# Kernel tuning notes

Hardware: AMD Instinct MI355X
Metric: run time of the kernel (lower is better)

Reference implementation:

```python
import jax, jax.numpy as jnp
import numpy as np

EPS = 1e-5


def setup_inputs() -> dict:
    key = jax.random.key(0)
    ks = jax.random.split(key, 14)
    N, C, H, W, D = 2048, 512, 4, 4, 64
    inp = {
        "x": jax.random.normal(ks[0], (N, C, H, W), jnp.float32),
        "W123": jax.random.normal(ks[1], (3, D, C), jnp.float32) * 0.05,
        "b123": jax.random.normal(ks[2], (3, D), jnp.float32) * 0.05,
        "g123": jax.random.uniform(ks[3], (3, D), jnp.float32, 0.5, 1.5),
        "be123": jax.random.normal(ks[4], (3, D), jnp.float32) * 0.05,
        "m123": jax.random.normal(ks[5], (3, D), jnp.float32) * 0.05,
        "v123": jax.random.uniform(ks[6], (3, D), jnp.float32, 0.5, 1.5),
        "W4": jax.random.normal(ks[7], (C, D), jnp.float32) * 0.05,
        "b4": jax.random.normal(ks[8], (C,), jnp.float32) * 0.05,
        "g4": jax.random.uniform(ks[9], (C,), jnp.float32, 0.5, 1.5),
        "be4": jax.random.normal(ks[10], (C,), jnp.float32) * 0.05,
        "m4": jax.random.normal(ks[11], (C,), jnp.float32) * 0.05,
        "v4": jax.random.uniform(ks[12], (C,), jnp.float32, 0.5, 1.5),
    }
    return inp


def reference(x, W123, b123, g123, be123, m123, v123, W4, b4, g4, be4, m4, v4):
    N, C, H, W = x.shape
    D = W123.shape[1]
    # three parallel 1x1 stride-2 conv branches == strided slice + channel GEMM
    xs = x[:, :, ::2, ::2]                                 # (N, C, H/2, W/2)
    proj = jnp.einsum('nchw,koc->knohw', xs, W123)         # (3, N, D, H/2, W/2)
    bcast = lambda p: p[:, None, :, None, None]
    bn = (proj + bcast(b123) - bcast(m123)) * (bcast(g123) / jnp.sqrt(bcast(v123) + EPS)) + bcast(be123)
    act = jax.nn.relu(bn)                                  # (3, N, D, h, w)
    L = act.shape[-2] * act.shape[-1]
    q = act[0].reshape(N, D, L).transpose(0, 2, 1)         # (N, L, D)
    k = act[1].reshape(N, D, L)                            # (N, D, L)
    v = act[2].reshape(N, D, L).transpose(0, 2, 1)         # (N, L, D)
    attn = jax.nn.softmax(jnp.einsum('nld,ndm->nlm', q, k), axis=2)  # (N, L, L)
    att = jnp.einsum('nlm,nmd->nld', attn, v).transpose(0, 2, 1)     # (N, D, L)
    att = att.reshape(N, D, W, -1)                         # (N, D, W, L//W)
    # conv2: 1x1 conv D->C + BN (no ReLU)
    out2 = jnp.einsum('ndhw,cd->nchw', att, W4) + b4[None, :, None, None]
    cb = lambda p: p[None, :, None, None]
    bn2 = (out2 - cb(m4)) * (cb(g4) / jnp.sqrt(cb(v4) + EPS)) + cb(be4)
    return x + bn2                                         # broadcasts (N,C,4,1) -> (N,C,4,4)
```

## Files before the change

kernel.cpp:

```cpp
#include <hip/hip_runtime.h>
#include <hip/hip_bf16.h>
#include <math.h>

#define EPS 1e-5f

typedef __attribute__((ext_vector_type(8))) short bf8_t;
typedef __attribute__((ext_vector_type(4))) float f4_t;

static __device__ __forceinline__ unsigned short f2b(float f) {
    __hip_bfloat16 h = __float2bfloat16(f);
    return *reinterpret_cast<unsigned short*>(&h);
}


__global__ __launch_bounds__(256) void k0_prep(
    const float* __restrict__ W123, const float* __restrict__ W4,
    const float* __restrict__ b123, const float* __restrict__ g123,
    const float* __restrict__ be123, const float* __restrict__ m123, const float* __restrict__ v123,
    const float* __restrict__ b4, const float* __restrict__ g4,
    const float* __restrict__ be4, const float* __restrict__ m4, const float* __restrict__ v4,
    unsigned short* __restrict__ w1b, unsigned short* __restrict__ w4b,
    float* __restrict__ bn1s, float* __restrict__ bn1h,
    float* __restrict__ bn2s, float* __restrict__ bn2h)
{
    const int bid = blockIdx.x, tid = threadIdx.x;
    if (bid == 64) {
        if (tid < 192) {
            float s = g123[tid] * rsqrtf(v123[tid] + EPS);
            bn1s[tid] = s;
            bn1h[tid] = be123[tid] + (b123[tid] - m123[tid]) * s;
        }
        for (int c = tid; c < 512; c += 256) {
            float s = g4[c] * rsqrtf(v4[c] + EPS);
            bn2s[c] = s;
            bn2h[c] = be4[c] + (b4[c] - m4[c]) * s;
        }
        return;
    }
    const int f = bid * 256 + tid;
    const float* src;
    unsigned short* dst;
    if (f < 12288) {
        int mt = f >> 10, ks = (f >> 6) & 15, lane = f & 63;
        int row = mt * 16 + (lane & 15);
        int k0  = ks * 32 + ((lane >> 4) << 3);
        src = W123 + row * 512 + k0;
        dst = w1b + f * 8;
    } else {
        int f2 = f - 12288;
        int mt = f2 >> 7, ks = (f2 >> 6) & 1, lane = f2 & 63;
        int row = mt * 16 + (lane & 15);
        int k0  = ks * 32 + ((lane >> 4) << 3);
        src = W4 + row * 64 + k0;
        dst = w4b + f2 * 8;
    }
    float4 a = *(const float4*)src;
    float4 b = *(const float4*)(src + 4);
    union { unsigned short u[8]; uint4 v; } o;
    o.u[0]=f2b(a.x); o.u[1]=f2b(a.y); o.u[2]=f2b(a.z); o.u[3]=f2b(a.w);
    o.u[4]=f2b(b.x); o.u[5]=f2b(b.y); o.u[6]=f2b(b.z); o.u[7]=f2b(b.w);
    *(uint4*)dst = o.v;
}

__global__ __launch_bounds__(256, 8) void k1_mfma(
    const float* __restrict__ x,
    const unsigned short* __restrict__ w1b,
    const unsigned short* __restrict__ w4b,
    const float* __restrict__ bn1s, const float* __restrict__ bn1h,
    const float* __restrict__ bn2s, const float* __restrict__ bn2h,
    float* __restrict__ out)
{
    __shared__ __align__(16) char U[8768];
    __shared__ float smx[20];

    unsigned short* Bxs  = (unsigned short*)&U[0];
    float*          actL = (float*)&U[4160];
    unsigned short* B2   = (unsigned short*)&U[0];
    float*          bn2L = (float*)&U[576];

    const int tid = threadIdx.x;
    const int lane = tid & 63, w = tid >> 6;
    const int n = blockIdx.x;
    const float4* x4 = (const float4*)(x + (size_t)n * 8192);
    float4* o4 = (float4*)(out + (size_t)n * 8192);

    #pragma unroll
    for (int k = 0; k < 8; ++k) {
        int f = tid + k * 256;
        float4 v = x4[f];
        int c = f >> 2, j = f & 3;
        if (j == 0) {
            Bxs[0 * 520 + c] = f2b(v.x);
            Bxs[1 * 520 + c] = f2b(v.z);
        } else if (j == 2) {
            Bxs[2 * 520 + c] = f2b(v.x);
            Bxs[3 * 520 + c] = f2b(v.z);
        }
    }
    __syncthreads();

    {
        f4_t acc[3] = {};
        const bf8_t* Af = (const bf8_t*)w1b;
        const int col = lane & 15, kb = (lane >> 4) << 3;
        for (int ks = 0; ks < 16; ++ks) {
            bf8_t bf = *(const bf8_t*)&Bxs[(col & 3) * 520 + ks * 32 + kb];
            #pragma unroll
            for (int mi = 0; mi < 3; ++mi) {
                int mt = w * 3 + mi;
                bf8_t af = Af[(mt * 16 + ks) * 64 + lane];
                acc[mi] = __builtin_amdgcn_mfma_f32_16x16x32_bf16(af, bf, acc[mi], 0, 0, 0);
            }
        }
        if (col < 4) {
            #pragma unroll
            for (int mi = 0; mi < 3; ++mi) {
                int rbase = (w * 3 + mi) * 16 + ((lane >> 4) << 2);
                #pragma unroll
                for (int r = 0; r < 4; ++r) {
                    int row = rbase + r;
                    float v = acc[mi][r] * bn1s[row] + bn1h[row];
                    actL[row * 5 + col] = fmaxf(v, 0.f);
                }
            }
        }
    }
    __syncthreads();

    if (tid < 32) {
        int l = (tid >> 3) & 3, m = (tid >> 1) & 3, dg = tid & 1;
        float part = 0.f;
        #pragma unroll 8
        for (int kk = 0; kk < 32; ++kk) {
            int d = dg * 32 + kk;
            part += actL[d * 5 + l] * actL[(64 + d) * 5 + m];
        }
        part += __shfl_xor(part, 1);
        if (dg == 0) smx[l * 4 + m] = part;
    }
    __syncthreads();

    if (tid < 4) {
        int l = tid;
        float s0 = smx[l*4+0], s1 = smx[l*4+1], s2 = smx[l*4+2], s3 = smx[l*4+3];
        float mx = fmaxf(fmaxf(s0, s1), fmaxf(s2, s3));
        float e0 = expf(s0-mx), e1 = expf(s1-mx), e2 = expf(s2-mx), e3 = expf(s3-mx);
        float inv = 1.f / (e0 + e1 + e2 + e3);
        smx[l*4+0] = e0*inv; smx[l*4+1] = e1*inv;
        smx[l*4+2] = e2*inv; smx[l*4+3] = e3*inv;
    }
    __syncthreads();

    if (tid < 32) {
        int l = tid >> 3, d0 = (tid & 7) * 8;
        float p0 = smx[l*4+0], p1 = smx[l*4+1], p2 = smx[l*4+2], p3 = smx[l*4+3];
        #pragma unroll
        for (int j = 0; j < 8; ++j) {
            int d = d0 + j;
            float sum = p0 * actL[(128+d)*5 + 0] + p1 * actL[(128+d)*5 + 1]
                      + p2 * actL[(128+d)*5 + 2] + p3 * actL[(128+d)*5 + 3];
            B2[l * 72 + d] = f2b(sum);
        }
    }
    __syncthreads();

    {
        const bf8_t* A2f = (const bf8_t*)w4b;
        const int col = lane & 15, kb = (lane >> 4) << 3;
        f4_t acc2[8] = {};
        #pragma unroll
        for (int ks = 0; ks < 2; ++ks) {
            bf8_t bf = *(const bf8_t*)&B2[(col & 3) * 72 + ks * 32 + kb];
            #pragma unroll
            for (int mi = 0; mi < 8; ++mi) {
                int mt = w * 8 + mi;
                bf8_t af = A2f[(mt * 2 + ks) * 64 + lane];
                acc2[mi] = __builtin_amdgcn_mfma_f32_16x16x32_bf16(af, bf, acc2[mi], 0, 0, 0);
            }
        }
        if (col < 4) {
            #pragma unroll
            for (int mi = 0; mi < 8; ++mi) {
                int cbase = (w * 8 + mi) * 16 + ((lane >> 4) << 2);
                #pragma unroll
                for (int r = 0; r < 4; ++r) {
                    int c = cbase + r;
                    bn2L[c * 4 + col] = acc2[mi][r] * bn2s[c] + bn2h[c];
                }
            }
        }
    }
    __syncthreads();

    #pragma unroll
    for (int k = 0; k < 8; ++k) {
        int f = tid + k * 256;
        int c = f >> 2, j = f & 3;
        float b = bn2L[c * 4 + j];
        float4 v = x4[f];
        o4[f] = make_float4(v.x + b, v.y + b, v.z + b, v.w + b);
    }
}

extern "C" void kernel_launch(void* const* d_in, const int* in_sizes, int n_in,
                              void* d_out, int out_size, void* d_ws, size_t ws_size,
                              hipStream_t stream) {
    const float* x     = (const float*)d_in[0];
    const float* W123  = (const float*)d_in[1];
    const float* b123  = (const float*)d_in[2];
    const float* g123  = (const float*)d_in[3];
    const float* be123 = (const float*)d_in[4];
    const float* m123  = (const float*)d_in[5];
    const float* v123  = (const float*)d_in[6];
    const float* W4    = (const float*)d_in[7];
    const float* b4    = (const float*)d_in[8];
    const float* g4    = (const float*)d_in[9];
    const float* be4   = (const float*)d_in[10];
    const float* m4    = (const float*)d_in[11];
    const float* v4    = (const float*)d_in[12];
    float* outp = (float*)d_out;

    char* ws = (char*)d_ws;
    unsigned short* w1b = (unsigned short*)ws;
    unsigned short* w4b = (unsigned short*)(ws + 196608);
    float* bn1s = (float*)(ws + 262144);
    float* bn1h = (float*)(ws + 262912);
    float* bn2s = (float*)(ws + 263680);
    float* bn2h = (float*)(ws + 265728);

    k0_prep<<<65, 256, 0, stream>>>(W123, W4, b123, g123, be123, m123, v123,
                                    b4, g4, be4, m4, v4,
                                    w1b, w4b, bn1s, bn1h, bn2s, bn2h);
    k1_mfma<<<2048, 256, 0, stream>>>(x, w1b, w4b, bn1s, bn1h, bn2s, bn2h, outp);
}
```

Before: 188.1 us.

## Keep x tile in registers and fuse attention softmax phases via shuffles

Each block now loads its x tile into registers once and reuses it for the final residual add instead of re-reading global memory. The score, softmax and weighted-sum phases are merged into one 64-thread wave using shuffles, which removes two block-wide barriers and the shared softmax buffer. Launch bounds drop from 8 to 4 waves per SIMD to leave room for the extra 32 registers, at the cost of lower occupancy. A partial unroll is also added to the first MFMA loop.

```diff
diff --git a/kernel.cpp b/kernel.cpp
--- a/kernel.cpp
+++ b/kernel.cpp
@@ -62,7 +62,7 @@
     *(uint4*)dst = o.v;
 }
 
-__global__ __launch_bounds__(256, 8) void k1_mfma(
+__global__ __launch_bounds__(256, 4) void k1_mfma(
     const float* __restrict__ x,
     const unsigned short* __restrict__ w1b,
     const unsigned short* __restrict__ w4b,
@@ -71,7 +71,6 @@
     float* __restrict__ out)
 {
     __shared__ __align__(16) char U[8768];
-    __shared__ float smx[20];
 
     unsigned short* Bxs  = (unsigned short*)&U[0];
     float*          actL = (float*)&U[4160];
@@ -84,17 +83,27 @@
     const float4* x4 = (const float4*)(x + (size_t)n * 8192);
     float4* o4 = (float4*)(out + (size_t)n * 8192);
 
+    float4 xr[8];
     #pragma unroll
-    for (int k = 0; k < 8; ++k) {
-        int f = tid + k * 256;
-        float4 v = x4[f];
-        int c = f >> 2, j = f & 3;
+    for (int k = 0; k < 8; ++k) xr[k] = x4[tid + k * 256];
+
+    {
+        const int j = tid & 3;
+        const int cb = tid >> 2;
         if (j == 0) {
-            Bxs[0 * 520 + c] = f2b(v.x);
-            Bxs[1 * 520 + c] = f2b(v.z);
+            #pragma unroll
+            for (int k = 0; k < 8; ++k) {
+                int c = cb + k * 64;
+                Bxs[0 * 520 + c] = f2b(xr[k].x);
+                Bxs[1 * 520 + c] = f2b(xr[k].z);
+            }
         } else if (j == 2) {
-            Bxs[2 * 520 + c] = f2b(v.x);
-            Bxs[3 * 520 + c] = f2b(v.z);
+            #pragma unroll
+            for (int k = 0; k < 8; ++k) {
+                int c = cb + k * 64;
+                Bxs[2 * 520 + c] = f2b(xr[k].x);
+                Bxs[3 * 520 + c] = f2b(xr[k].z);
+            }
         }
     }
     __syncthreads();
@@ -103,6 +112,7 @@
         f4_t acc[3] = {};
         const bf8_t* Af = (const bf8_t*)w1b;
         const int col = lane & 15, kb = (lane >> 4) << 3;
+        #pragma unroll 4
         for (int ks = 0; ks < 16; ++ks) {
             bf8_t bf = *(const bf8_t*)&Bxs[(col & 3) * 520 + ks * 32 + kb];
             #pragma unroll
@@ -127,39 +137,34 @@
     }
     __syncthreads();
 
-    if (tid < 32) {
-        int l = (tid >> 3) & 3, m = (tid >> 1) & 3, dg = tid & 1;
+    if (tid < 64) {
+        int i = (tid & 31) >> 1, dg = tid & 1;
+        int sl = i >> 2, sm = i & 3;
         float part = 0.f;
         #pragma unroll 8
         for (int kk = 0; kk < 32; ++kk) {
             int d = dg * 32 + kk;
-            part += actL[d * 5 + l] * actL[(64 + d) * 5 + m];
+            part += actL[d * 5 + sl] * actL[(64 + d) * 5 + sm];
         }
         part += __shfl_xor(part, 1);
-        if (dg == 0) smx[l * 4 + m] = part;
-    }
-    __syncthreads();
-
-    if (tid < 4) {
-        int l = tid;
-        float s0 = smx[l*4+0], s1 = smx[l*4+1], s2 = smx[l*4+2], s3 = smx[l*4+3];
+
+        int l2 = tid >> 4, dblk = tid & 15;
+        float s0 = __shfl(part, (l2 * 4 + 0) * 2);
+        float s1 = __shfl(part, (l2 * 4 + 1) * 2);
+        float s2 = __shfl(part, (l2 * 4 + 2) * 2);
+        float s3 = __shfl(part, (l2 * 4 + 3) * 2);
         float mx = fmaxf(fmaxf(s0, s1), fmaxf(s2, s3));
-        float e0 = expf(s0-mx), e1 = expf(s1-mx), e2 = expf(s2-mx), e3 = expf(s3-mx);
+        float e0 = expf(s0 - mx), e1 = expf(s1 - mx);
+        float e2 = expf(s2 - mx), e3 = expf(s3 - mx);
         float inv = 1.f / (e0 + e1 + e2 + e3);
-        smx[l*4+0] = e0*inv; smx[l*4+1] = e1*inv;
-        smx[l*4+2] = e2*inv; smx[l*4+3] = e3*inv;
-    }
-    __syncthreads();
-
-    if (tid < 32) {
-        int l = tid >> 3, d0 = (tid & 7) * 8;
-        float p0 = smx[l*4+0], p1 = smx[l*4+1], p2 = smx[l*4+2], p3 = smx[l*4+3];
+        float p0 = e0 * inv, p1 = e1 * inv, p2 = e2 * inv, p3 = e3 * inv;
+
         #pragma unroll
-        for (int j = 0; j < 8; ++j) {
-            int d = d0 + j;
-            float sum = p0 * actL[(128+d)*5 + 0] + p1 * actL[(128+d)*5 + 1]
-                      + p2 * actL[(128+d)*5 + 2] + p3 * actL[(128+d)*5 + 3];
-            B2[l * 72 + d] = f2b(sum);
+        for (int jj = 0; jj < 4; ++jj) {
+            int d = dblk * 4 + jj;
+            float sum = p0 * actL[(128 + d) * 5 + 0] + p1 * actL[(128 + d) * 5 + 1]
+                      + p2 * actL[(128 + d) * 5 + 2] + p3 * actL[(128 + d) * 5 + 3];
+            B2[l2 * 72 + d] = f2b(sum);
         }
     }
     __syncthreads();
@@ -195,10 +200,8 @@
     #pragma unroll
     for (int k = 0; k < 8; ++k) {
         int f = tid + k * 256;
-        int c = f >> 2, j = f & 3;
-        float b = bn2L[c * 4 + j];
-        float4 v = x4[f];
-        o4[f] = make_float4(v.x + b, v.y + b, v.z + b, v.w + b);
+        float b = bn2L[f];
+        o4[f] = make_float4(xr[k].x + b, xr[k].y + b, xr[k].z + b, xr[k].w + b);
     }
 }
 
```

Measured after the change: 154.9 us. -17.7%, faster.
